# Performance work log

Measured on AMD Instinct MI355X. Metric: run time of the kernel, lower is better.

The kernel has to match this reference:

```python
import jax, jax.numpy as jnp
import numpy as np

N_NEURONS = 50000
N_BKG = 100
N_SYN_BASIS = 5
N_EDGES = 500000
BATCH = 1
SEQ_T = 250
BKG_RATE_PROB = 0.25  # bkg_firing_rate(250) * 0.001


def setup_inputs() -> dict:
    key = jax.random.key(0)
    k_w, k_tau, k_sp, k_r, k_c = jax.random.split(key, 5)
    weights = jax.random.normal(k_w, (N_EDGES,), dtype=jnp.float32)
    tau_syn = jax.random.uniform(k_tau, (N_EDGES, N_SYN_BASIS), dtype=jnp.float32)
    # Bernoulli background spikes, shape [B*T, n_bkg_units]
    spikes = (jax.random.uniform(k_sp, (BATCH * SEQ_T, N_BKG)) < BKG_RATE_PROB).astype(jnp.float32)
    rows = jax.random.randint(k_r, (N_EDGES,), 0, N_NEURONS, dtype=jnp.int32)
    cols = jax.random.randint(k_c, (N_EDGES,), 0, N_BKG, dtype=jnp.int32)
    return {"weights": weights, "tau_syn": tau_syn, "spikes": spikes,
            "rows": rows, "cols": cols}


def reference(weights, tau_syn, spikes, rows, cols):
    # Per-receptor edge values: weights[e] * tau_syn[e, r]  -> [E, R]
    vals = weights[:, None] * tau_syn
    # Densify the (identical-structure) sparse matrix once for all receptors;
    # duplicate (row, col) indices accumulate, matching tf.sparse semantics
    # used through sparse_dense_matmul. W: [N, K, R]
    W = jnp.zeros((N_NEURONS, N_BKG, N_SYN_BASIS), dtype=spikes.dtype).at[rows, cols].add(vals)
    # i_receptor[r] = sparse_w_in @ spikes.T -> stacked [R, N, BT];
    # tf.transpose reverses axes -> [BT, N, R]; fused here as one einsum.
    out = jnp.einsum('nkr,bk->bnr', W, spikes)  # [BT, N, R]
    return out.reshape(BATCH, SEQ_T, N_NEURONS * N_SYN_BASIS)
```

## Files before the change

kernel.cpp:

```cpp
#include <hip/hip_runtime.h>


#define N_NEURONS 50000
#define N_BKG     100
#define N_SYN     5
#define N_EDGES   500000
#define SEQ_T     250
#define NCOL      (N_NEURONS * N_SYN)
#define RPB       16
#define NBINS     (N_NEURONS / RPB)
#define NPART     8
#define CAP_P     64
#define RECS_BIN  (NPART * CAP_P)
#define KPAD      128
#define CPADF     80
#define BCOLS     80
#define NXCD      8

#define LDS_BYTES 32000

#define WS_COUNT_OFF 0
#define WS_SPB_OFF   131072
#define WS_REC_OFF   262144

typedef __attribute__((ext_vector_type(8))) short bf16x8;
typedef __attribute__((ext_vector_type(4))) float f32x4;

__device__ inline unsigned short bf16_rne(float f) {
    unsigned u = __builtin_bit_cast(unsigned, f);
    u += 0x7FFFu + ((u >> 16) & 1u);
    return (unsigned short)(u >> 16);
}
__device__ inline float bf16_up(unsigned hw) {
    return __builtin_bit_cast(float, hw << 16);
}

__global__ __launch_bounds__(256) void bucket_kernel(
        const float* __restrict__ weights,
        const float* __restrict__ tau,
        const int*   __restrict__ rows,
        const int*   __restrict__ cols,
        const float* __restrict__ spikes,
        unsigned* __restrict__ count,
        uint4* __restrict__ rec,
        bf16x8* __restrict__ spbf) {
    int gid = blockIdx.x * 256 + threadIdx.x;
    if (gid < 4096) {
        int lane = gid & 63;
        int kk   = (gid >> 6) & 3;
        int nt   = gid >> 8;
        int t    = nt * 16 + (lane & 15);
        int k0   = kk * 32 + (lane >> 4) * 8;
        bf16x8 v;
#pragma unroll
        for (int i = 0; i < 8; ++i) {
            float s = 0.f;
            if (t < SEQ_T && (k0 + i) < N_BKG)
                s = spikes[t * N_BKG + k0 + i];
            v[i] = (short)bf16_rne(s);
        }
        spbf[gid] = v;
    }
    if (gid >= N_EDGES) return;
    int row = rows[gid];
    int col = cols[gid];
    float w = weights[gid];
    const float* tp = tau + (size_t)gid * N_SYN;
    int bin  = row >> 4;
    int part = blockIdx.x & (NPART - 1);
    unsigned slot = atomicAdd(&count[bin * NPART + part], 1u);
    if (slot >= CAP_P) return;
    uint4 r;
    r.x = ((unsigned)col << 4) | (unsigned)(row & 15);
    r.y = (unsigned)bf16_rne(w * tp[0]) | ((unsigned)bf16_rne(w * tp[1]) << 16);
    r.z = (unsigned)bf16_rne(w * tp[2]) | ((unsigned)bf16_rne(w * tp[3]) << 16);
    r.w = (unsigned)bf16_rne(w * tp[4]);
    rec[(size_t)bin * RECS_BIN + part * CAP_P + slot] = r;
}

__global__ __launch_bounds__(256, 4) void fused_kernel(
        const unsigned* __restrict__ count,
        const uint4* __restrict__ rec,
        const bf16x8* __restrict__ spbf,
        float* __restrict__ out) {
    __shared__ __align__(16) char lds[LDS_BYTES];
    float* slice = (float*)lds;

    const int tid = threadIdx.x;
    const int l   = tid & 63;
    const int wv  = tid >> 6;
    const int lc  = l & 15;
    const int lq  = l >> 4;

    const int orig = blockIdx.x;
    const int xcd  = orig & (NXCD - 1);
    const int q    = NBINS >> 3;
    const int r8   = NBINS & 7;
    const int bin  = (xcd < r8 ? xcd * (q + 1)
                               : r8 * (q + 1) + (xcd - r8) * q) + (orig >> 3);

    const uint4* rbin = rec + (size_t)bin * RECS_BIN;
    unsigned cntA = count[bin * NPART + wv];
    unsigned cntB = count[bin * NPART + 4 + wv];
    if (cntA > CAP_P) cntA = CAP_P;
    if (cntB > CAP_P) cntB = CAP_P;
    uint4 ra = rbin[wv * CAP_P + l];
    uint4 rb = rbin[(4 + wv) * CAP_P + l];
    bool havea = (unsigned)l < cntA;
    bool haveb = (unsigned)l < cntB;

    bf16x8 bs[4][4];
#pragma unroll
    for (int n = 0; n < 4; ++n)
#pragma unroll
        for (int kk = 0; kk < 4; ++kk)
            bs[n][kk] = spbf[((wv * 4 + n) * 4 + kk) * 64 + l];

    {
        f32x4* s4 = (f32x4*)lds;
        f32x4 z = (f32x4){0.f, 0.f, 0.f, 0.f};
#pragma unroll
        for (int j = 0; j < 8; ++j) {
            int i = tid + j * 256;
            if (i < 2000) s4[i] = z;
        }
    }
    __syncthreads();

    if (havea) {
        float* base = &slice[(ra.x >> 4) * CPADF + (ra.x & 15u) * N_SYN];
        atomicAdd(base + 0, bf16_up(ra.y & 0xFFFFu));
        atomicAdd(base + 1, bf16_up(ra.y >> 16));
        atomicAdd(base + 2, bf16_up(ra.z & 0xFFFFu));
        atomicAdd(base + 3, bf16_up(ra.z >> 16));
        atomicAdd(base + 4, bf16_up(ra.w & 0xFFFFu));
    }
    if (haveb) {
        float* base = &slice[(rb.x >> 4) * CPADF + (rb.x & 15u) * N_SYN];
        atomicAdd(base + 0, bf16_up(rb.y & 0xFFFFu));
        atomicAdd(base + 1, bf16_up(rb.y >> 16));
        atomicAdd(base + 2, bf16_up(rb.z & 0xFFFFu));
        atomicAdd(base + 3, bf16_up(rb.z >> 16));
        atomicAdd(base + 4, bf16_up(rb.w & 0xFFFFu));
    }
    __syncthreads();

    bf16x8 hi[5];
    unsigned bo[5];
#pragma unroll
    for (int j = 0; j < 5; ++j) {
        int m  = tid + j * 256;
        int c  = m % BCOLS;
        int kb = m / BCOLS;
#pragma unroll
        for (int i = 0; i < 8; ++i) {
            int k = kb * 8 + i;
            float v = (k < N_BKG) ? slice[k * CPADF + c] : 0.f;
            hi[j][i] = (short)bf16_rne(v);
        }
        bo[j] = (unsigned)(((c << 8) + (kb << 4)) ^ ((c & 7) << 4));
    }
    __syncthreads();
#pragma unroll
    for (int j = 0; j < 5; ++j)
        *(bf16x8*)(lds + bo[j]) = hi[j];
    __syncthreads();

    const size_t cb = (size_t)bin * BCOLS;
#pragma unroll
    for (int m = 0; m < 5; ++m) {
        f32x4 acc[4];
#pragma unroll
        for (int n = 0; n < 4; ++n)
            acc[n] = (f32x4){0.f, 0.f, 0.f, 0.f};

        int c = m * 16 + lc;
#pragma unroll
        for (int kk = 0; kk < 4; ++kk) {
            int bor = (((c << 8) + (kk << 6) + (lq << 4)) ^ ((c & 7) << 4));
            bf16x8 ah = *(const bf16x8*)(lds + bor);
#pragma unroll
            for (int n = 0; n < 4; ++n)
                acc[n] = __builtin_amdgcn_mfma_f32_16x16x32_bf16(
                             ah, bs[n][kk], acc[n], 0, 0, 0);
        }
        size_t cs = cb + m * 16 + lq * 4;
#pragma unroll
        for (int n = 0; n < 4; ++n) {
            int t = (wv * 4 + n) * 16 + lc;
            if (t < SEQ_T)
                *(f32x4*)(out + (size_t)t * NCOL + cs) = acc[n];
        }
    }
}

extern "C" void kernel_launch(void* const* d_in, const int* in_sizes, int n_in,
                              void* d_out, int out_size, void* d_ws, size_t ws_size,
                              hipStream_t stream) {
    const float* weights = (const float*)d_in[0];
    const float* tau     = (const float*)d_in[1];
    const float* spikes  = (const float*)d_in[2];
    const int*   rows    = (const int*)d_in[3];
    const int*   cols    = (const int*)d_in[4];
    float* out = (float*)d_out;

    char* ws = (char*)d_ws;
    unsigned* count = (unsigned*)(ws + WS_COUNT_OFF);
    bf16x8*   spbf  = (bf16x8*)(ws + WS_SPB_OFF);
    uint4*    rec   = (uint4*)(ws + WS_REC_OFF);

    hipMemsetAsync(count, 0, NBINS * NPART * sizeof(unsigned), stream);

    int eblocks = (N_EDGES + 255) / 256;
    bucket_kernel<<<eblocks, 256, 0, stream>>>(weights, tau, rows, cols, spikes,
                                               count, rec, spbf);

    fused_kernel<<<NBINS, 256, 0, stream>>>(count, rec, spbf, out);
}
```

Baseline: 119.6 us.

## Transpose bucket counters, stride bin order within XCD, defer spike fragment loads

The per-bin partition counters are laid out partition-major instead of bin-major, so atomics from different partitions land on separate cache lines. Bins within each XCD's contiguous range are visited with a stride of 37 modulo the range size, which scatters concurrently running blocks across the output and the record buffer. The spike B-fragment loads move to after the LDS scatter, which shortens their register live range during the atomic phase. The stride permutation makes output writes less sequential and may hurt DRAM locality.

After: 112.6 us. 5.9% less time.

```diff
diff --git a/kernel.cpp b/kernel.cpp
--- a/kernel.cpp
+++ b/kernel.cpp
@@ -12,10 +12,9 @@
 #define NPART     8
 #define CAP_P     64
 #define RECS_BIN  (NPART * CAP_P)
-#define KPAD      128
 #define CPADF     80
 #define BCOLS     80
-#define NXCD      8
+#define STRIDE_J  37
 
 #define LDS_BYTES 32000
 
@@ -68,7 +67,7 @@
     const float* tp = tau + (size_t)gid * N_SYN;
     int bin  = row >> 4;
     int part = blockIdx.x & (NPART - 1);
-    unsigned slot = atomicAdd(&count[bin * NPART + part], 1u);
+    unsigned slot = atomicAdd(&count[part * NBINS + bin], 1u);
     if (slot >= CAP_P) return;
     uint4 r;
     r.x = ((unsigned)col << 4) | (unsigned)(row & 15);
@@ -93,15 +92,15 @@
     const int lq  = l >> 4;
 
     const int orig = blockIdx.x;
-    const int xcd  = orig & (NXCD - 1);
-    const int q    = NBINS >> 3;
-    const int r8   = NBINS & 7;
-    const int bin  = (xcd < r8 ? xcd * (q + 1)
-                               : r8 * (q + 1) + (xcd - r8) * q) + (orig >> 3);
+    const int xcd  = orig & 7;
+    const int j    = orig >> 3;
+    const int qx   = (xcd < 5) ? 391 : 390;
+    const int base = (xcd < 5) ? xcd * 391 : 5 * 391 + (xcd - 5) * 390;
+    const int bin  = base + (j * STRIDE_J) % qx;
 
     const uint4* rbin = rec + (size_t)bin * RECS_BIN;
-    unsigned cntA = count[bin * NPART + wv];
-    unsigned cntB = count[bin * NPART + 4 + wv];
+    unsigned cntA = count[wv * NBINS + bin];
+    unsigned cntB = count[(4 + wv) * NBINS + bin];
     if (cntA > CAP_P) cntA = CAP_P;
     if (cntB > CAP_P) cntB = CAP_P;
     uint4 ra = rbin[wv * CAP_P + l];
@@ -109,61 +108,64 @@
     bool havea = (unsigned)l < cntA;
     bool haveb = (unsigned)l < cntB;
 
-    bf16x8 bs[4][4];
-#pragma unroll
-    for (int n = 0; n < 4; ++n)
-#pragma unroll
-        for (int kk = 0; kk < 4; ++kk)
-            bs[n][kk] = spbf[((wv * 4 + n) * 4 + kk) * 64 + l];
-
     {
         f32x4* s4 = (f32x4*)lds;
         f32x4 z = (f32x4){0.f, 0.f, 0.f, 0.f};
 #pragma unroll
-        for (int j = 0; j < 8; ++j) {
-            int i = tid + j * 256;
+        for (int jj = 0; jj < 8; ++jj) {
+            int i = tid + jj * 256;
             if (i < 2000) s4[i] = z;
         }
     }
     __syncthreads();
 
     if (havea) {
-        float* base = &slice[(ra.x >> 4) * CPADF + (ra.x & 15u) * N_SYN];
-        atomicAdd(base + 0, bf16_up(ra.y & 0xFFFFu));
-        atomicAdd(base + 1, bf16_up(ra.y >> 16));
-        atomicAdd(base + 2, bf16_up(ra.z & 0xFFFFu));
-        atomicAdd(base + 3, bf16_up(ra.z >> 16));
-        atomicAdd(base + 4, bf16_up(ra.w & 0xFFFFu));
+        float* bp = &slice[(ra.x >> 4) * CPADF + (ra.x & 15u) * N_SYN];
+        atomicAdd(bp + 0, bf16_up(ra.y & 0xFFFFu));
+        atomicAdd(bp + 1, bf16_up(ra.y >> 16));
+        atomicAdd(bp + 2, bf16_up(ra.z & 0xFFFFu));
+        atomicAdd(bp + 3, bf16_up(ra.z >> 16));
+        atomicAdd(bp + 4, bf16_up(ra.w & 0xFFFFu));
     }
     if (haveb) {
-        float* base = &slice[(rb.x >> 4) * CPADF + (rb.x & 15u) * N_SYN];
-        atomicAdd(base + 0, bf16_up(rb.y & 0xFFFFu));
-        atomicAdd(base + 1, bf16_up(rb.y >> 16));
-        atomicAdd(base + 2, bf16_up(rb.z & 0xFFFFu));
-        atomicAdd(base + 3, bf16_up(rb.z >> 16));
-        atomicAdd(base + 4, bf16_up(rb.w & 0xFFFFu));
+        float* bp = &slice[(rb.x >> 4) * CPADF + (rb.x & 15u) * N_SYN];
+        atomicAdd(bp + 0, bf16_up(rb.y & 0xFFFFu));
+        atomicAdd(bp + 1, bf16_up(rb.y >> 16));
+        atomicAdd(bp + 2, bf16_up(rb.z & 0xFFFFu));
+        atomicAdd(bp + 3, bf16_up(rb.z >> 16));
+        atomicAdd(bp + 4, bf16_up(rb.w & 0xFFFFu));
     }
     __syncthreads();
 
     bf16x8 hi[5];
-    unsigned bo[5];
-#pragma unroll
-    for (int j = 0; j < 5; ++j) {
-        int m  = tid + j * 256;
+#pragma unroll
+    for (int jj = 0; jj < 5; ++jj) {
+        int m  = tid + jj * 256;
         int c  = m % BCOLS;
         int kb = m / BCOLS;
 #pragma unroll
         for (int i = 0; i < 8; ++i) {
             int k = kb * 8 + i;
             float v = (k < N_BKG) ? slice[k * CPADF + c] : 0.f;
-            hi[j][i] = (short)bf16_rne(v);
-        }
-        bo[j] = (unsigned)(((c << 8) + (kb << 4)) ^ ((c & 7) << 4));
-    }
-    __syncthreads();
-#pragma unroll
-    for (int j = 0; j < 5; ++j)
-        *(bf16x8*)(lds + bo[j]) = hi[j];
+            hi[jj][i] = (short)bf16_rne(v);
+        }
+    }
+    __syncthreads();
+#pragma unroll
+    for (int jj = 0; jj < 5; ++jj) {
+        int m  = tid + jj * 256;
+        int c  = m % BCOLS;
+        int kb = m / BCOLS;
+        unsigned bo = (unsigned)(((c << 8) + (kb << 4)) ^ ((c & 7) << 4));
+        *(bf16x8*)(lds + bo) = hi[jj];
+    }
+
+    bf16x8 bs[4][4];
+#pragma unroll
+    for (int n = 0; n < 4; ++n)
+#pragma unroll
+        for (int kk = 0; kk < 4; ++kk)
+            bs[n][kk] = spbf[((wv * 4 + n) * 4 + kk) * 64 + l];
     __syncthreads();
 
     const size_t cb = (size_t)bin * BCOLS;
@@ -209,7 +211,7 @@
     bf16x8*   spbf  = (bf16x8*)(ws + WS_SPB_OFF);
     uint4*    rec   = (uint4*)(ws + WS_REC_OFF);
 
-    hipMemsetAsync(count, 0, NBINS * NPART * sizeof(unsigned), stream);
+    hipMemsetAsync(count, 0, NPART * NBINS * sizeof(unsigned), stream);
 
     int eblocks = (N_EDGES + 255) / 256;
     bucket_kernel<<<eblocks, 256, 0, stream>>>(weights, tau, rows, cols, spikes,
```
